# Kernel tuning notes

Hardware: AMD Instinct MI355X
Metric: run time of the kernel (lower is better)

The kernel has to match this reference:

```python
import jax, jax.numpy as jnp
import numpy as np
from jax import lax

H = W = 496
K = 5            # gabor kernel size
WIN = 16         # window_size
STRIDE = 16
PATCH = 32
GAMMA = 0.5
PSI = np.pi / 2
THETAS = np.array([np.pi/8, np.pi/4, 3*np.pi/8, np.pi/2, 5*np.pi/8, 6*np.pi/8, 7*np.pi/8, np.pi], dtype=np.float32)


def setup_inputs() -> dict:
    key = jax.random.key(0)
    k1, k2, k3 = jax.random.split(key, 3)
    img = jax.random.normal(k1, (1, 1, H, W), dtype=jnp.float32)
    sigmas = jax.random.uniform(k2, (1, 3), dtype=jnp.float32) * 10.0   # nn.Parameter(rand*10)
    lambdas = jax.random.uniform(k3, (1, 3), dtype=jnp.float32) * np.pi  # nn.Parameter(rand*pi)
    return {"img": img, "sigmas": sigmas, "lambdas": lambdas}


def _gabor_bank(sigmas, lambdas):
    # axes: (sigma, lambda, theta, ky, kx)
    idx = jnp.arange(K, dtype=jnp.float32) - (K - 1) / 2.0
    sig = sigmas[0][:, None, None, None, None]          # [3,1,1,1,1]
    lam = lambdas[0][None, :, None, None, None]         # [1,3,1,1,1]
    th = jnp.asarray(THETAS)[None, None, :, None, None] # [1,1,8,1,1]
    y = idx[None, None, None, :, None]
    x = idx[None, None, None, None, :]
    sigma_x = sig
    sigma_y = sig / GAMMA
    sin_t, cos_t = jnp.sin(th), jnp.cos(th)
    y_theta = -x * sin_t + y * cos_t
    x_theta = x * cos_t + y * sin_t
    gb = jnp.exp(-0.5 * (x_theta**2 / sigma_x**2 + y_theta**2 / sigma_y**2)) \
         * jnp.cos(2.0 * np.pi * x_theta / lam + PSI)
    return gb.reshape(-1, 1, K, K)  # [72,1,5,5]


def reference(img, sigmas, lambdas):
    gb = _gabor_bank(sigmas, lambdas)
    res = lax.conv_general_dilated(
        img, gb, window_strides=(1, 1), padding=[(K // 2, K // 2)] * 2,
        dimension_numbers=("NCHW", "OIHW", "NCHW"))          # [1,72,H,W]
    res = res.reshape(1, 9, 8, H, W).max(axis=2)              # max over 8 thetas -> [1,9,H,W]
    out = res[0]                                              # [9,H,W]

    # find_maxima: per-channel threshold at 5*mean, zero below (torch.nn.Threshold)
    mean = out.mean(axis=(1, 2), keepdims=True)
    thr = jnp.where(out > mean * 5.0, out, 0.0)

    nw = H // STRIDE                                          # 31
    windows = thr.reshape(9, nw, WIN, nw, WIN).transpose(0, 1, 3, 2, 4).reshape(9, nw * nw, WIN * WIN)
    is_max = jnp.argmax(windows, axis=2) == (WIN * WIN) // 2  # [9, 961]

    w_idx = jnp.arange(nw * nw)
    rows = w_idx // nw * STRIDE + WIN // 2
    cols = w_idx % nw * STRIDE + WIN // 2

    # describe: zero-pad by 16, gather 32x32 patch at each candidate keypoint for every channel
    pad = jnp.pad(out, ((0, 0), (16, 16), (16, 16)))
    pr = rows[:, None, None] + jnp.arange(PATCH)[None, :, None]   # [961,32,1]
    pc = cols[:, None, None] + jnp.arange(PATCH)[None, None, :]   # [961,1,32]
    patches = pad[:, pr, pc]                                      # [9,961,32,32]

    # keep patches only for detected keypoints with nonzero content (original skips zero patches)
    valid_kp = jnp.any(is_max, axis=0)                            # [961]
    nonzero = jnp.any(patches != 0, axis=(2, 3))                  # [9,961]
    mask = (valid_kp[None, :] & nonzero).astype(patches.dtype)
    patches = patches * mask[:, :, None, None]
    return patches
```

## Files before the change

### kernel.cpp

```cpp
#include <hip/hip_runtime.h>
#include <math.h>

#define HH 496
#define WW 496
#define HWSZ (HH*WW)
#define NW 31
#define NWIN (NW*NW)

__constant__ float c_thetas[8] = {
    0.39269908169872414f, 0.7853981633974483f, 1.1780972450961724f,
    1.5707963267948966f,  1.9634954084936207f, 2.356194490192345f,
    2.748893571891069f,   3.141592653589793f};

__global__ void bank_kernel(const float* __restrict__ sigmas,
                            const float* __restrict__ lambdas,
                            float* __restrict__ filt) {
    int idx = threadIdx.x + blockIdx.x * blockDim.x;
    if (idx >= 72 * 25) return;
    int f = idx / 25, k = idx % 25;
    int dy = k / 5, dx = k % 5;
    int s = f / 24, rem = f % 24, l = rem / 8, t = rem % 8;
    float sig = sigmas[s], lam = lambdas[l], th = c_thetas[t];
    float y = (float)dy - 2.0f, x = (float)dx - 2.0f;
    float st = sinf(th), ct = cosf(th);
    float yt = -x * st + y * ct;
    float xt =  x * ct + y * st;
    float sx2 = sig * sig;
    float sy2 = 4.0f * sig * sig;
    float g = expf(-0.5f * (xt * xt / sx2 + yt * yt / sy2)) *
              cosf(6.28318530717958647692f * xt / lam + 1.5707963267948966f);
    filt[idx] = g;
}

__global__ __launch_bounds__(256) void conv_kernel(
    const float* __restrict__ img, const float* __restrict__ filt,
    float* __restrict__ out, float* __restrict__ partial) {
    __shared__ float tile[20 * 20];
    __shared__ float red[4];
    int tid = threadIdx.x;
    int tx = tid & 15, ty = tid >> 4;
    int bx = blockIdx.x, by = blockIdx.y;

    for (int i = tid; i < 400; i += 256) {
        int tY = i / 20, tX = i % 20;
        int gy = by * 16 + tY - 2, gx = bx * 16 + tX - 2;
        float v = 0.0f;
        if (gy >= 0 && gy < HH && gx >= 0 && gx < WW) v = img[gy * WW + gx];
        tile[i] = v;
    }
    __syncthreads();

    float r[25];
#pragma unroll
    for (int dy = 0; dy < 5; dy++)
#pragma unroll
        for (int dx = 0; dx < 5; dx++)
            r[dy * 5 + dx] = tile[(ty + dy) * 20 + (tx + dx)];

    int y = by * 16 + ty, x = bx * 16 + tx;

    for (int c = 0; c < 9; c++) {
        float maxv = -3.402823466e38f;
#pragma unroll
        for (int t = 0; t < 8; t++) {
            const float* fp = filt + (c * 8 + t) * 25;
            float acc = 0.0f;
#pragma unroll
            for (int k = 0; k < 25; k++) acc += r[k] * fp[k];
            maxv = fmaxf(maxv, acc);
        }
        out[c * HWSZ + y * WW + x] = maxv;

        float s = maxv;
#pragma unroll
        for (int off = 32; off > 0; off >>= 1) s += __shfl_down(s, off, 64);
        if ((tid & 63) == 0) red[tid >> 6] = s;
        __syncthreads();
        if (tid == 0)
            partial[(by * NW + bx) * 9 + c] = red[0] + red[1] + red[2] + red[3];
        __syncthreads();
    }
}

__global__ void mean_kernel(const float* __restrict__ partial,
                            float* __restrict__ mean) {
    __shared__ float red[256];
    int tid = threadIdx.x;
    for (int c = 0; c < 9; c++) {
        float s = 0.0f;
        for (int i = tid; i < NWIN; i += 256) s += partial[i * 9 + c];
        red[tid] = s;
        __syncthreads();
        for (int off = 128; off > 0; off >>= 1) {
            if (tid < off) red[tid] += red[tid + off];
            __syncthreads();
        }
        if (tid == 0) mean[c] = red[0] * (1.0f / (float)HWSZ);
        __syncthreads();
    }
}

__global__ __launch_bounds__(256) void patch_kernel(
    const float* __restrict__ out, const float* __restrict__ mean,
    float* __restrict__ dst) {
    int w = blockIdx.x;
    int r = w / NW, cl = w % NW;
    int tid = threadIdx.x;
    int wy = tid >> 4, wx = tid & 15;
    __shared__ float centerv;

    bool valid = false;
    for (int c = 0; c < 9; c++) {
        float v = out[c * HWSZ + (r * 16 + wy) * WW + (cl * 16 + wx)];
        float m5 = mean[c] * 5.0f;
        float thr = (v > m5) ? v : 0.0f;
        if (tid == 128) centerv = thr;
        __syncthreads();
        float cv = centerv;
        bool ok = (tid < 128) ? (thr < cv) : ((tid > 128) ? (thr <= cv) : true);
        int all = __syncthreads_and(ok ? 1 : 0);
        if (all) valid = true;
    }

    for (int c = 0; c < 9; c++) {
        float vals[4];
        bool nzl = false;
#pragma unroll
        for (int q = 0; q < 4; q++) {
            int e = q * 256 + tid;
            int i = e >> 5, j = e & 31;
            int row = r * 16 + i - 8;
            int col = cl * 16 + j - 8;
            float v = 0.0f;
            if (row >= 0 && row < HH && col >= 0 && col < WW)
                v = out[c * HWSZ + row * WW + col];
            vals[q] = v;
            nzl = nzl || (v != 0.0f);
        }
        int nz = __syncthreads_or(nzl ? 1 : 0);
        float mk = (valid && nz) ? 1.0f : 0.0f;
#pragma unroll
        for (int q = 0; q < 4; q++) {
            int e = q * 256 + tid;
            dst[(size_t)c * NWIN * 1024 + (size_t)w * 1024 + e] = vals[q] * mk;
        }
    }
}

extern "C" void kernel_launch(void* const* d_in, const int* in_sizes, int n_in,
                              void* d_out, int out_size, void* d_ws, size_t ws_size,
                              hipStream_t stream) {
    const float* img     = (const float*)d_in[0];
    const float* sigmas  = (const float*)d_in[1];
    const float* lambdas = (const float*)d_in[2];
    float* ws = (float*)d_ws;
    float* filt    = ws;
    float* partial = ws + 2048;
    float* meanp   = ws + 11008;
    float* outb    = ws + 11264;

    bank_kernel<<<8, 256, 0, stream>>>(sigmas, lambdas, filt);
    conv_kernel<<<dim3(NW, NW), 256, 0, stream>>>(img, filt, outb, partial);
    mean_kernel<<<1, 256, 0, stream>>>(partial, meanp);
    patch_kernel<<<NWIN, 256, 0, stream>>>(outb, meanp, (float*)d_out);
}
```

Baseline: 131.2 us.

## Replace mean kernel with atomics and batch block-level reductions into bitmasks

Drops the separate single-block mean kernel: conv blocks now atomically add their per-channel sums into padded accumulators that the bank kernel zeroes. Inside conv the nine per-channel block syncs are replaced by one sync after all channels are reduced. The patch kernel builds per-channel bitmasks for the argmax-at-centre test and the nonzero test, reduces them with wave shuffles and a single barrier, and loads all nine channels before writing. The cost is nondeterministic float atomic ordering in the mean and more registers in the patch kernel.

```diff
diff --git a/kernel.cpp b/kernel.cpp
--- a/kernel.cpp
+++ b/kernel.cpp
@@ -14,9 +14,13 @@
 
 __global__ void bank_kernel(const float* __restrict__ sigmas,
                             const float* __restrict__ lambdas,
-                            float* __restrict__ filt) {
+                            float* __restrict__ filt,
+                            float* __restrict__ meanacc) {
     int idx = threadIdx.x + blockIdx.x * blockDim.x;
-    if (idx >= 72 * 25) return;
+    if (idx >= 1800) {
+        if (idx < 1809) meanacc[(idx - 1800) * 16] = 0.0f;
+        return;
+    }
     int f = idx / 25, k = idx % 25;
     int dy = k / 5, dx = k % 5;
     int s = f / 24, rem = f % 24, l = rem / 8, t = rem % 8;
@@ -34,9 +38,9 @@
 
 __global__ __launch_bounds__(256) void conv_kernel(
     const float* __restrict__ img, const float* __restrict__ filt,
-    float* __restrict__ out, float* __restrict__ partial) {
+    float* __restrict__ out, float* __restrict__ meanacc) {
     __shared__ float tile[20 * 20];
-    __shared__ float red[4];
+    __shared__ float red[4][9];
     int tid = threadIdx.x;
     int tx = tid & 15, ty = tid >> 4;
     int bx = blockIdx.x, by = blockIdx.y;
@@ -59,6 +63,8 @@
 
     int y = by * 16 + ty, x = bx * 16 + tx;
 
+    float sums[9];
+#pragma unroll
     for (int c = 0; c < 9; c++) {
         float maxv = -3.402823466e38f;
 #pragma unroll
@@ -70,61 +76,51 @@
             maxv = fmaxf(maxv, acc);
         }
         out[c * HWSZ + y * WW + x] = maxv;
+        sums[c] = maxv;
+    }
 
-        float s = maxv;
+#pragma unroll
+    for (int c = 0; c < 9; c++) {
+        float s = sums[c];
 #pragma unroll
         for (int off = 32; off > 0; off >>= 1) s += __shfl_down(s, off, 64);
-        if ((tid & 63) == 0) red[tid >> 6] = s;
-        __syncthreads();
-        if (tid == 0)
-            partial[(by * NW + bx) * 9 + c] = red[0] + red[1] + red[2] + red[3];
-        __syncthreads();
+        if ((tid & 63) == 0) red[tid >> 6][c] = s;
     }
-}
-
-__global__ void mean_kernel(const float* __restrict__ partial,
-                            float* __restrict__ mean) {
-    __shared__ float red[256];
-    int tid = threadIdx.x;
-    for (int c = 0; c < 9; c++) {
-        float s = 0.0f;
-        for (int i = tid; i < NWIN; i += 256) s += partial[i * 9 + c];
-        red[tid] = s;
-        __syncthreads();
-        for (int off = 128; off > 0; off >>= 1) {
-            if (tid < off) red[tid] += red[tid + off];
-            __syncthreads();
-        }
-        if (tid == 0) mean[c] = red[0] * (1.0f / (float)HWSZ);
-        __syncthreads();
-    }
+    __syncthreads();
+    if (tid < 9)
+        atomicAdd(&meanacc[tid * 16],
+                  red[0][tid] + red[1][tid] + red[2][tid] + red[3][tid]);
 }
 
 __global__ __launch_bounds__(256) void patch_kernel(
-    const float* __restrict__ out, const float* __restrict__ mean,
+    const float* __restrict__ out, const float* __restrict__ meanacc,
     float* __restrict__ dst) {
     int w = blockIdx.x;
     int r = w / NW, cl = w % NW;
     int tid = threadIdx.x;
     int wy = tid >> 4, wx = tid & 15;
-    __shared__ float centerv;
+    __shared__ int lds_and[4];
+    __shared__ int lds_or[4];
 
-    bool valid = false;
+    int okmask = 0;
+#pragma unroll
     for (int c = 0; c < 9; c++) {
-        float v = out[c * HWSZ + (r * 16 + wy) * WW + (cl * 16 + wx)];
-        float m5 = mean[c] * 5.0f;
-        float thr = (v > m5) ? v : 0.0f;
-        if (tid == 128) centerv = thr;
-        __syncthreads();
-        float cv = centerv;
-        bool ok = (tid < 128) ? (thr < cv) : ((tid > 128) ? (thr <= cv) : true);
-        int all = __syncthreads_and(ok ? 1 : 0);
-        if (all) valid = true;
+        float m5 = meanacc[c * 16] * (5.0f / (float)HWSZ);
+        float v  = out[c * HWSZ + (r * 16 + wy) * WW + (cl * 16 + wx)];
+        float vc = out[c * HWSZ + (r * 16 + 8) * WW + (cl * 16 + 0)];
+        float thr  = (v  > m5) ? v  : 0.0f;
+        float thrc = (vc > m5) ? vc : 0.0f;
+        bool ok = (tid < 128) ? (thr < thrc) : (thr <= thrc);
+        okmask |= (ok ? 1 : 0) << c;
     }
+#pragma unroll
+    for (int off = 1; off < 64; off <<= 1) okmask &= __shfl_xor(okmask, off, 64);
+    if ((tid & 63) == 0) lds_and[tid >> 6] = okmask;
 
+    float vals[9][4];
+    int nzmask = 0;
+#pragma unroll
     for (int c = 0; c < 9; c++) {
-        float vals[4];
-        bool nzl = false;
 #pragma unroll
         for (int q = 0; q < 4; q++) {
             int e = q * 256 + tid;
@@ -134,15 +130,26 @@
             float v = 0.0f;
             if (row >= 0 && row < HH && col >= 0 && col < WW)
                 v = out[c * HWSZ + row * WW + col];
-            vals[q] = v;
-            nzl = nzl || (v != 0.0f);
+            vals[c][q] = v;
+            if (v != 0.0f) nzmask |= 1 << c;
         }
-        int nz = __syncthreads_or(nzl ? 1 : 0);
-        float mk = (valid && nz) ? 1.0f : 0.0f;
+    }
+#pragma unroll
+    for (int off = 1; off < 64; off <<= 1) nzmask |= __shfl_xor(nzmask, off, 64);
+    if ((tid & 63) == 0) lds_or[tid >> 6] = nzmask;
+    __syncthreads();
+
+    int am = lds_and[0] & lds_and[1] & lds_and[2] & lds_and[3];
+    int om = lds_or[0] | lds_or[1] | lds_or[2] | lds_or[3];
+    bool valid = (am != 0);
+
+#pragma unroll
+    for (int c = 0; c < 9; c++) {
+        float mk = (valid && ((om >> c) & 1)) ? 1.0f : 0.0f;
 #pragma unroll
         for (int q = 0; q < 4; q++) {
             int e = q * 256 + tid;
-            dst[(size_t)c * NWIN * 1024 + (size_t)w * 1024 + e] = vals[q] * mk;
+            dst[(size_t)c * NWIN * 1024 + (size_t)w * 1024 + e] = vals[c][q] * mk;
         }
     }
 }
@@ -155,12 +162,10 @@
     const float* lambdas = (const float*)d_in[2];
     float* ws = (float*)d_ws;
     float* filt    = ws;
-    float* partial = ws + 2048;
-    float* meanp   = ws + 11008;
-    float* outb    = ws + 11264;
+    float* meanacc = ws + 2048;
+    float* outb    = ws + 4096;
 
-    bank_kernel<<<8, 256, 0, stream>>>(sigmas, lambdas, filt);
-    conv_kernel<<<dim3(NW, NW), 256, 0, stream>>>(img, filt, outb, partial);
-    mean_kernel<<<1, 256, 0, stream>>>(partial, meanp);
-    patch_kernel<<<NWIN, 256, 0, stream>>>(outb, meanp, (float*)d_out);
+    bank_kernel<<<8, 256, 0, stream>>>(sigmas, lambdas, filt, meanacc);
+    conv_kernel<<<dim3(NW, NW), 256, 0, stream>>>(img, filt, outb, meanacc);
+    patch_kernel<<<NWIN, 256, 0, stream>>>(outb, meanacc, (float*)d_out);
 }
```

Result: slower. 134.4 us (+2.4%).
